# Performance work log

Measured on AMD Instinct MI355X. Metric: run time of the kernel, lower is better.

## Reference

```python
import jax, jax.numpy as jnp
import numpy as np

N, E, DIN, H, L, NCLS = 50000, 800000, 256, 384, 6, 2
EPS = 1e-5

def setup_inputs() -> dict:
    key = jax.random.key(0)
    ks = jax.random.split(key, 24)
    def lin(k, fan_in, shape):
        b = 1.0 / np.sqrt(fan_in)
        return jax.random.uniform(k, shape, jnp.float32, -b, b)
    inp = {}
    inp['x'] = jax.random.normal(ks[0], (N, DIN), jnp.float32)
    inp['edge_index'] = jax.random.randint(ks[1], (2, E), 0, N, jnp.int32)
    inp['W_in'] = lin(ks[2], DIN, (DIN, H)); inp['b_in'] = lin(ks[3], DIN, (H,))
    inp['bn0_g'] = jnp.ones((H,), jnp.float32); inp['bn0_b'] = jnp.zeros((H,), jnp.float32)
    inp['Wl'] = lin(ks[4], H, (L, H, H)); inp['bl'] = lin(ks[5], H, (L, H))
    inp['Wr'] = lin(ks[6], H, (L, H, H))
    inp['bn_g'] = jnp.ones((L, H), jnp.float32); inp['bn_b'] = jnp.zeros((L, H), jnp.float32)
    inp['Wskip'] = lin(ks[7], H, (L // 2, H, H)); inp['bskip'] = lin(ks[8], H, (L // 2, H))
    inp['W1'] = lin(ks[9], H, (H, H // 2)); inp['b1'] = lin(ks[10], H, (H // 2,))
    inp['W2'] = lin(ks[11], H // 2, (H // 2, H // 4)); inp['b2'] = lin(ks[12], H // 2, (H // 4,))
    inp['W3'] = lin(ks[13], H // 4, (H // 4, NCLS)); inp['b3'] = lin(ks[14], H // 4, (NCLS,))
    return inp

def _batchnorm(h, g, b):
    mu = jnp.mean(h, axis=0)
    var = jnp.mean(jnp.square(h - mu), axis=0)  # biased, as torch BN training
    return (h - mu) * jax.lax.rsqrt(var + EPS) * g + b

def reference(x, edge_index, W_in, b_in, bn0_g, bn0_b, Wl, bl, Wr, bn_g, bn_b,
              Wskip, bskip, W1, b1, W2, b2, W3, b3):
    row, col = edge_index[0], edge_index[1]  # messages flow row -> col
    cnt = jax.ops.segment_sum(jnp.ones((E,), jnp.float32), col, num_segments=N)
    inv_cnt = (1.0 / jnp.maximum(cnt, 1.0))[:, None]  # [N,1]

    h = _batchnorm(x @ W_in + b_in, bn0_g, bn0_b)
    h = jax.nn.relu(h)  # dropout is identity in eval

    skip_idx = 0
    for i in range(L):
        identity = h
        agg = jax.ops.segment_sum(h[row], col, num_segments=N) * inv_cnt  # mean aggregation
        h = agg @ Wl[i] + bl[i] + h @ Wr[i]  # SAGEConv: lin_l(mean) + lin_r(x)
        h = jax.nn.relu(_batchnorm(h, bn_g[i], bn_b[i]))
        if (i + 1) % 2 == 0 and skip_idx < L // 2:
            h = h + identity @ Wskip[skip_idx] + bskip[skip_idx]
            skip_idx += 1

    embeddings = h
    h = jax.nn.relu(h @ W1 + b1)
    h = jax.nn.relu(h @ W2 + b2)
    out = h @ W3 + b3
    return (out, embeddings)
```

## Files before the change

### kernel.cpp

```cpp
#include <hip/hip_runtime.h>

#define H 384
#define EPS 1e-5f

typedef __attribute__((ext_vector_type(8))) short bf8v;
typedef __attribute__((ext_vector_type(8))) unsigned short us8;
typedef __attribute__((ext_vector_type(4))) float f32x4;

__device__ __forceinline__ float b2f(unsigned short b) {
    return __builtin_bit_cast(float, (unsigned)b << 16);
}
__device__ __forceinline__ unsigned short f2b(float f) {
    unsigned u = __builtin_bit_cast(unsigned, f);
    u += 0x7FFFu + ((u >> 16) & 1u);
    return (unsigned short)(u >> 16);
}
__device__ __forceinline__ float u2f_lo(unsigned u) {
    return __builtin_bit_cast(float, u << 16);
}
__device__ __forceinline__ float u2f_hi(unsigned u) {
    return __builtin_bit_cast(float, u & 0xFFFF0000u);
}

__device__ __forceinline__ void gload16(const unsigned short* g, unsigned short* l) {
    __builtin_amdgcn_global_load_lds(
        (const __attribute__((address_space(1))) void*)g,
        (__attribute__((address_space(3))) void*)l, 16, 0, 0);
}

__global__ __launch_bounds__(256) void gemm_mfma(
    const unsigned short* __restrict__ A1, const unsigned short* __restrict__ W1t,
    const unsigned short* __restrict__ A2, const unsigned short* __restrict__ W2t,
    const float* __restrict__ bias, unsigned short* __restrict__ Cb,
    float* __restrict__ bnsum, float* __restrict__ bnsq,
    int Nr, int K, int M, int relu)
{
    __shared__ unsigned short smem[17408];
    __shared__ float s_stat[256];
    unsigned short* sA = smem;
    unsigned short* sB = smem + 8192;
    const int t = threadIdx.x;
    const int wave = t >> 6, lane = t & 63;
    const int wr = (wave >> 1) * 64, wc = (wave & 1) * 64;
    const int c0 = blockIdx.x * 128, r0 = blockIdx.y * 128;
    const int lm = lane & 15, lq = lane >> 4;
    const int l8 = lane >> 3;
    const int gsw8 = ((lane & 7) ^ l8) * 8;
    f32x4 acc[4][4] = {};

    s_stat[t] = 0.f;

    const int npass = (A2 != nullptr) ? 2 : 1;
    for (int pass = 0; pass < npass; ++pass) {
        const unsigned short* __restrict__ A = pass ? A2 : A1;
        const unsigned short* __restrict__ W = pass ? W2t : W1t;
        for (int k0 = 0; k0 < K; k0 += 64) {
            #pragma unroll
            for (int s = 0; s < 4; ++s) {
                const int seg = (wave << 2) + s;
                const int tr = (seg << 3) + l8;
                int gr = r0 + tr; if (gr >= Nr) gr = Nr - 1;
                gload16(A + (long)gr * K + k0 + gsw8, sA + (seg << 9));
                int gc = c0 + tr; if (gc >= M) gc = M - 1;
                gload16(W + (long)gc * K + k0 + gsw8, sB + (seg << 9));
            }
            __syncthreads();
            #pragma unroll
            for (int kk = 0; kk < 2; ++kk) {
                const int pc = (((kk << 2) | lq) ^ (lm & 7)) << 3;
                bf8v af[4], bf[4];
                #pragma unroll
                for (int i = 0; i < 4; ++i) {
                    const int ra = wr + (i << 4) + lm;
                    af[i] = *(const bf8v*)(sA + (ra << 6) + pc);
                    const int rb = wc + (i << 4) + lm;
                    bf[i] = *(const bf8v*)(sB + (rb << 6) + pc);
                }
                #pragma unroll
                for (int i = 0; i < 4; ++i)
                    #pragma unroll
                    for (int j = 0; j < 4; ++j)
                        acc[i][j] = __builtin_amdgcn_mfma_f32_16x16x32_bf16(
                            af[i], bf[j], acc[i][j], 0, 0, 0);
            }
            __syncthreads();
        }
    }

    const bool do_stats = (bnsum != nullptr);
    unsigned short* sC = smem;

    #pragma unroll
    for (int j = 0; j < 4; ++j) {
        const int lcol = wc + (j << 4) + lm;
        const int col = c0 + lcol;
        const float bi = (col < M) ? bias[col] : 0.f;
        float ls = 0.f, lss = 0.f;
        #pragma unroll
        for (int i = 0; i < 4; ++i) {
            const int lrow = wr + (i << 4) + (lq << 2);
            #pragma unroll
            for (int r = 0; r < 4; ++r) {
                float v = acc[i][j][r] + bi;
                if (r0 + lrow + r < Nr) { ls += v; lss += v * v; }
                sC[(lrow + r) * 136 + lcol] = f2b(relu ? fmaxf(v, 0.f) : v);
            }
        }
        if (do_stats && col < M) {
            atomicAdd(&s_stat[lcol], ls);
            atomicAdd(&s_stat[128 + lcol], lss);
        }
    }
    __syncthreads();
    if (do_stats && t < 128) {
        int col = c0 + t;
        if (col < M) {
            atomicAdd(&bnsum[col], s_stat[t]);
            atomicAdd(&bnsq[col], s_stat[128 + t]);
        }
    }
    #pragma unroll
    for (int it = 0; it < 8; ++it) {
        const int idx = (it << 8) + t;
        const int lrow = idx >> 4;
        const int ch = idx & 15;
        const int rowg = r0 + lrow;
        const int col = c0 + (ch << 3);
        if (rowg < Nr && col < M)
            *(bf8v*)(Cb + (long)rowg * M + col) =
                *(const bf8v*)(sC + lrow * 136 + (ch << 3));
    }
}

__global__ void wt_convert(const float* __restrict__ W, unsigned short* __restrict__ Wt,
                           int total, int K, int M)
{
    int idx = blockIdx.x * 256 + threadIdx.x;
    if (idx >= total) return;
    int l = idx / (K * M), rem = idx - l * K * M;
    int k = rem / M, m = rem - k * M;
    Wt[(long)l * K * M + (long)m * K + k] = f2b(W[idx]);
}

__global__ void f2b_vec(const float* __restrict__ X, unsigned short* __restrict__ Y, int n4)
{
    int idx = blockIdx.x * 256 + threadIdx.x;
    if (idx >= n4) return;
    float4 v = *(const float4*)(X + idx * 4);
    ushort4 o = {f2b(v.x), f2b(v.y), f2b(v.z), f2b(v.w)};
    *(ushort4*)(Y + idx * 4) = o;
}

__global__ void count_edges_i(const int* __restrict__ col, int* __restrict__ cnt, int E)
{
    int e = blockIdx.x * 256 + threadIdx.x;
    if (e < E) atomicAdd(&cnt[col[e]], 1);
}

__global__ __launch_bounds__(1024) void exscan_csr(const int* __restrict__ cnt,
                                                   int* __restrict__ offs, int n)
{
    __shared__ int s[1024];
    const int t = threadIdx.x;
    const int chunk = (n + 1023) >> 10;
    int lo = t * chunk, hi = lo + chunk;
    if (lo > n) lo = n;
    if (hi > n) hi = n;
    int sum = 0;
    for (int i = lo; i < hi; ++i) sum += cnt[i];
    s[t] = sum;
    __syncthreads();
    for (int d = 1; d < 1024; d <<= 1) {
        int o = (t >= d) ? s[t - d] : 0;
        __syncthreads();
        s[t] += o;
        __syncthreads();
    }
    int base = (t == 0) ? 0 : s[t - 1];
    for (int i = lo; i < hi; ++i) { offs[i] = base; base += cnt[i]; }
    if (t == 1023) offs[n] = s[1023];
}

__global__ void fill_csr(const int* __restrict__ row, const int* __restrict__ col,
                         const int* __restrict__ offs, int* __restrict__ cursor,
                         int* __restrict__ csr_rows, int E)
{
    int e = blockIdx.x * 256 + threadIdx.x;
    if (e < E) {
        int c = col[e];
        int p = offs[c] + atomicAdd(&cursor[c], 1);
        csr_rows[p] = row[e];
    }
}

__global__ void inv_from_cnt(const int* __restrict__ cnt, float* __restrict__ inv, int n)
{
    int i = blockIdx.x * 256 + threadIdx.x;
    if (i < n) inv[i] = 1.0f / fmaxf((float)cnt[i], 1.0f);
}

__global__ __launch_bounds__(256) void agg_gather(
    const unsigned short* __restrict__ hb, const int* __restrict__ csr_rows,
    const int* __restrict__ offs, const float* __restrict__ inv,
    unsigned short* __restrict__ aggb, int N)
{
    const int wave = threadIdx.x >> 6, lane = threadIdx.x & 63;
    const int node = blockIdx.x * 4 + wave;
    if (node >= N) return;
    const int lo = offs[node], hi = offs[node + 1];
    const int lofs = lane * 6;
    float s0 = 0.f, s1 = 0.f, s2 = 0.f, s3 = 0.f, s4 = 0.f, s5 = 0.f;
    int e = lo;
    for (; e + 7 < hi; e += 8) {
        uint3 v[8];
        #pragma unroll
        for (int q = 0; q < 8; ++q) {
            int r = __builtin_amdgcn_readfirstlane(csr_rows[e + q]);
            v[q] = *(const uint3*)(hb + (long)r * H + lofs);
        }
        #pragma unroll
        for (int q = 0; q < 8; ++q) {
            s0 += u2f_lo(v[q].x); s1 += u2f_hi(v[q].x);
            s2 += u2f_lo(v[q].y); s3 += u2f_hi(v[q].y);
            s4 += u2f_lo(v[q].z); s5 += u2f_hi(v[q].z);
        }
    }
    for (; e + 3 < hi; e += 4) {
        uint3 v[4];
        #pragma unroll
        for (int q = 0; q < 4; ++q) {
            int r = __builtin_amdgcn_readfirstlane(csr_rows[e + q]);
            v[q] = *(const uint3*)(hb + (long)r * H + lofs);
        }
        #pragma unroll
        for (int q = 0; q < 4; ++q) {
            s0 += u2f_lo(v[q].x); s1 += u2f_hi(v[q].x);
            s2 += u2f_lo(v[q].y); s3 += u2f_hi(v[q].y);
            s4 += u2f_lo(v[q].z); s5 += u2f_hi(v[q].z);
        }
    }
    for (; e < hi; ++e) {
        int r = __builtin_amdgcn_readfirstlane(csr_rows[e]);
        uint3 v = *(const uint3*)(hb + (long)r * H + lofs);
        s0 += u2f_lo(v.x); s1 += u2f_hi(v.x);
        s2 += u2f_lo(v.y); s3 += u2f_hi(v.y);
        s4 += u2f_lo(v.z); s5 += u2f_hi(v.z);
    }
    const float sc = inv[node];
    uint3 o;
    o.x = (unsigned)f2b(s0 * sc) | ((unsigned)f2b(s1 * sc) << 16);
    o.y = (unsigned)f2b(s2 * sc) | ((unsigned)f2b(s3 * sc) << 16);
    o.z = (unsigned)f2b(s4 * sc) | ((unsigned)f2b(s5 * sc) << 16);
    *(uint3*)(aggb + (long)node * H + lofs) = o;
}

__global__ __launch_bounds__(256) void bn_apply(
    const unsigned short* __restrict__ X, const float* __restrict__ bnsum,
    const float* __restrict__ bnsq, const float* __restrict__ g,
    const float* __restrict__ b, const unsigned short* __restrict__ S,
    unsigned short* __restrict__ outb, float* __restrict__ outf,
    int Nr, int total4)
{
    __shared__ float sc[H], sh[H];
    const int t = threadIdx.x;
    for (int j = t; j < H; j += 256) {
        float mu  = bnsum[j] / (float)Nr;
        float var = bnsq[j] / (float)Nr - mu * mu;
        float s   = g[j] * rsqrtf(fmaxf(var, 0.f) + EPS);
        sc[j] = s;
        sh[j] = b[j] - mu * s;
    }
    __syncthreads();
    int idx = blockIdx.x * 256 + t;
    if (idx >= total4) return;
    int base = idx * 4;
    int j = base % H;
    ushort4 v = *(const ushort4*)(X + base);
    float o0 = fmaxf(b2f(v.x) * sc[j + 0] + sh[j + 0], 0.f);
    float o1 = fmaxf(b2f(v.y) * sc[j + 1] + sh[j + 1], 0.f);
    float o2 = fmaxf(b2f(v.z) * sc[j + 2] + sh[j + 2], 0.f);
    float o3 = fmaxf(b2f(v.w) * sc[j + 3] + sh[j + 3], 0.f);
    if (S) {
        ushort4 s4 = *(const ushort4*)(S + base);
        o0 += b2f(s4.x); o1 += b2f(s4.y); o2 += b2f(s4.z); o3 += b2f(s4.w);
    }
    ushort4 o = {f2b(o0), f2b(o1), f2b(o2), f2b(o3)};
    *(ushort4*)(outb + base) = o;
    if (outf) {
        float4 of = {o0, o1, o2, o3};
        *(float4*)(outf + base) = of;
    }
}

__global__ void mlp3(const unsigned short* __restrict__ m2, const float* __restrict__ W3,
                     const float* __restrict__ b3, float* __restrict__ out, int N)
{
    int n = blockIdx.x * 256 + threadIdx.x;
    if (n >= N) return;
    float a0 = b3[0], a1 = b3[1];
    const unsigned short* r = m2 + (long)n * 96;
    #pragma unroll 4
    for (int k = 0; k < 96; ++k) {
        float v = b2f(r[k]);
        a0 += v * W3[k * 2];
        a1 += v * W3[k * 2 + 1];
    }
    out[n * 2 + 0] = a0;
    out[n * 2 + 1] = a1;
}

extern "C" void kernel_launch(void* const* d_in, const int* in_sizes, int n_in,
                              void* d_out, int out_size, void* d_ws, size_t ws_size,
                              hipStream_t stream)
{
    const float* x     = (const float*)d_in[0];
    const int*   ei    = (const int*)d_in[1];
    const float* W_in  = (const float*)d_in[2];
    const float* b_in  = (const float*)d_in[3];
    const float* bn0_g = (const float*)d_in[4];
    const float* bn0_b = (const float*)d_in[5];
    const float* Wl    = (const float*)d_in[6];
    const float* bl    = (const float*)d_in[7];
    const float* Wr    = (const float*)d_in[8];
    const float* bn_g  = (const float*)d_in[9];
    const float* bn_b  = (const float*)d_in[10];
    const float* Wskip = (const float*)d_in[11];
    const float* bskip = (const float*)d_in[12];
    const float* W1    = (const float*)d_in[13];
    const float* b1    = (const float*)d_in[14];
    const float* W2    = (const float*)d_in[15];
    const float* b2    = (const float*)d_in[16];
    const float* W3    = (const float*)d_in[17];
    const float* b3    = (const float*)d_in[18];

    const int DIN = 256;
    const int N = in_sizes[0] / DIN;
    const int E = in_sizes[1] / 2;
    const int* row = ei;
    const int* col = ei + E;
    const long NH = (long)N * H;

    unsigned short* tmp      = (unsigned short*)d_ws;
    unsigned short* hb       = tmp + NH;
    unsigned short* aggb     = hb + NH;
    unsigned short* Sbuf     = aggb + NH;
    unsigned short* xb       = Sbuf + NH;
    unsigned short* Wint     = xb + (long)N * DIN;
    unsigned short* Wlt      = Wint + (long)H * DIN;
    unsigned short* Wrt      = Wlt + 6L * H * H;
    unsigned short* Wskipt   = Wrt + 6L * H * H;
    unsigned short* W1t      = Wskipt + 3L * H * H;
    unsigned short* W2t      = W1t + 192L * H;
    float*          inv      = (float*)(W2t + 96L * 192);
    int*            offs     = (int*)(inv + N);
    int*            csr_rows = offs + (N + 1);
    int*            cnt      = csr_rows + E;
    int*            cursor   = cnt + N;
    float*          stats    = (float*)(cursor + N);
    float* out = (float*)d_out;
    float* emb = out + (long)N * 2;

    dim3 blk(256);
    const int rg128 = (N + 127) / 128;
    const int app_grid = (int)((NH / 4 + 255) / 256);

    hipMemsetAsync(cnt, 0, (2L * N + 14 * H) * sizeof(float), stream);

    count_edges_i<<<(E + 255) / 256, blk, 0, stream>>>(col, cnt, E);
    exscan_csr<<<1, 1024, 0, stream>>>(cnt, offs, N);
    inv_from_cnt<<<(N + 255) / 256, blk, 0, stream>>>(cnt, inv, N);
    fill_csr<<<(E + 255) / 256, blk, 0, stream>>>(row, col, offs, cursor, csr_rows, E);

    {
        int n1 = H * DIN;
        wt_convert<<<(n1 + 255) / 256, blk, 0, stream>>>(W_in, Wint, n1, DIN, H);
        int n2 = 6 * H * H;
        wt_convert<<<(n2 + 255) / 256, blk, 0, stream>>>(Wl, Wlt, n2, H, H);
        wt_convert<<<(n2 + 255) / 256, blk, 0, stream>>>(Wr, Wrt, n2, H, H);
        int n3 = 3 * H * H;
        wt_convert<<<(n3 + 255) / 256, blk, 0, stream>>>(Wskip, Wskipt, n3, H, H);
        int n4 = H * 192;
        wt_convert<<<(n4 + 255) / 256, blk, 0, stream>>>(W1, W1t, n4, H, 192);
        int n5 = 192 * 96;
        wt_convert<<<(n5 + 255) / 256, blk, 0, stream>>>(W2, W2t, n5, 192, 96);
    }

    {
        int n4 = N * DIN / 4;
        f2b_vec<<<(n4 + 255) / 256, blk, 0, stream>>>(x, xb, n4);
    }
    gemm_mfma<<<dim3(3, rg128), blk, 0, stream>>>(
        xb, Wint, nullptr, nullptr, b_in, tmp, stats, stats + H, N, DIN, H, 0);
    bn_apply<<<app_grid, blk, 0, stream>>>(
        tmp, stats, stats + H, bn0_g, bn0_b, nullptr, hb, nullptr, N, (int)(NH / 4));

    int skip_idx = 0;
    for (int i = 0; i < 6; ++i) {
        float* bs = stats + (i + 1) * 2 * H;
        agg_gather<<<(N + 3) / 4, blk, 0, stream>>>(hb, csr_rows, offs, inv, aggb, N);

        gemm_mfma<<<dim3(3, rg128), blk, 0, stream>>>(
            aggb, Wlt + (long)i * H * H, hb, Wrt + (long)i * H * H,
            bl + i * H, tmp, bs, bs + H, N, H, H, 0);

        const unsigned short* S = nullptr;
        if ((i & 1) == 1) {
            gemm_mfma<<<dim3(3, rg128), blk, 0, stream>>>(
                hb, Wskipt + (long)skip_idx * H * H, nullptr, nullptr,
                bskip + skip_idx * H, Sbuf, nullptr, nullptr, N, H, H, 0);
            skip_idx++;
            S = Sbuf;
        }
        bn_apply<<<app_grid, blk, 0, stream>>>(
            tmp, bs, bs + H, bn_g + i * H, bn_b + i * H, S, hb,
            (i == 5) ? emb : nullptr, N, (int)(NH / 4));
    }

    unsigned short* m1b = aggb;
    unsigned short* m2b = tmp;
    gemm_mfma<<<dim3(2, rg128), blk, 0, stream>>>(
        hb, W1t, nullptr, nullptr, b1, m1b, nullptr, nullptr, N, H, 192, 1);
    gemm_mfma<<<dim3(1, rg128), blk, 0, stream>>>(
        m1b, W2t, nullptr, nullptr, b2, m2b, nullptr, nullptr, N, 192, 96, 1);
    mlp3<<<(N + 255) / 256, blk, 0, stream>>>(m2b, W3, b3, out, N);
}
```

Baseline: 1.512 ms.

## Double-buffer GEMM k-tiles in LDS and vectorize final MLP layer loads

The MFMA GEMM moves from a single 64-wide k-tile buffer with two barriers per step to a double-buffered 32-wide k-tile pipeline. The next tile's global->LDS load is issued before computing the current one, with one barrier per step and a new XOR swizzle for the 32-column layout. The aim is to hide global load latency behind MFMA work, at the cost of twice as many loop iterations. Separately, mlp3 now caches W3 in shared memory and reads each row with 16-byte vector loads instead of scalar loads.

```diff
diff --git a/kernel.cpp b/kernel.cpp
--- a/kernel.cpp
+++ b/kernel.cpp
@@ -37,54 +37,56 @@
 {
     __shared__ unsigned short smem[17408];
     __shared__ float s_stat[256];
-    unsigned short* sA = smem;
-    unsigned short* sB = smem + 8192;
     const int t = threadIdx.x;
     const int wave = t >> 6, lane = t & 63;
     const int wr = (wave >> 1) * 64, wc = (wave & 1) * 64;
     const int c0 = blockIdx.x * 128, r0 = blockIdx.y * 128;
     const int lm = lane & 15, lq = lane >> 4;
-    const int l8 = lane >> 3;
-    const int gsw8 = ((lane & 7) ^ l8) * 8;
     f32x4 acc[4][4] = {};
 
     s_stat[t] = 0.f;
 
-    const int npass = (A2 != nullptr) ? 2 : 1;
-    for (int pass = 0; pass < npass; ++pass) {
-        const unsigned short* __restrict__ A = pass ? A2 : A1;
-        const unsigned short* __restrict__ W = pass ? W2t : W1t;
-        for (int k0 = 0; k0 < K; k0 += 64) {
+    const int K32 = K >> 5;
+    const int S = ((A2 != nullptr) ? 2 : 1) * K32;
+
+    auto stage = [&](int s, int b) {
+        const unsigned short* __restrict__ Ap = (s >= K32) ? A2 : A1;
+        const unsigned short* __restrict__ Wp = (s >= K32) ? W2t : W1t;
+        const int k0 = ((s >= K32) ? s - K32 : s) << 5;
+        unsigned short* Ab = smem + (b << 13);
+        #pragma unroll
+        for (int q = 0; q < 2; ++q) {
+            const int blk = (wave << 1) + q;
+            const int tr = (blk << 4) + (lane >> 2);
+            const int lc8 = (((lane & 3) ^ ((tr >> 1) & 3)) << 3);
+            int gr = r0 + tr; if (gr >= Nr) gr = Nr - 1;
+            gload16(Ap + (long)gr * K + k0 + lc8, Ab + (blk << 9));
+            int gc = c0 + tr; if (gc >= M) gc = M - 1;
+            gload16(Wp + (long)gc * K + k0 + lc8, Ab + 4096 + (blk << 9));
+        }
+    };
+
+    stage(0, 0);
+    __syncthreads();
+    for (int s = 0; s < S; ++s) {
+        const int cb = s & 1;
+        if (s + 1 < S) stage(s + 1, cb ^ 1);
+        const unsigned short* Ab = smem + (cb << 13);
+        bf8v af[4], bf[4];
+        #pragma unroll
+        for (int i = 0; i < 4; ++i) {
+            const int ra = wr + (i << 4) + lm;
+            af[i] = *(const bf8v*)(Ab + (ra << 5) + ((lq ^ ((ra >> 1) & 3)) << 3));
+            const int rb = wc + (i << 4) + lm;
+            bf[i] = *(const bf8v*)(Ab + 4096 + (rb << 5) + ((lq ^ ((rb >> 1) & 3)) << 3));
+        }
+        #pragma unroll
+        for (int i = 0; i < 4; ++i)
             #pragma unroll
-            for (int s = 0; s < 4; ++s) {
-                const int seg = (wave << 2) + s;
-                const int tr = (seg << 3) + l8;
-                int gr = r0 + tr; if (gr >= Nr) gr = Nr - 1;
-                gload16(A + (long)gr * K + k0 + gsw8, sA + (seg << 9));
-                int gc = c0 + tr; if (gc >= M) gc = M - 1;
-                gload16(W + (long)gc * K + k0 + gsw8, sB + (seg << 9));
-            }
-            __syncthreads();
-            #pragma unroll
-            for (int kk = 0; kk < 2; ++kk) {
-                const int pc = (((kk << 2) | lq) ^ (lm & 7)) << 3;
-                bf8v af[4], bf[4];
-                #pragma unroll
-                for (int i = 0; i < 4; ++i) {
-                    const int ra = wr + (i << 4) + lm;
-                    af[i] = *(const bf8v*)(sA + (ra << 6) + pc);
-                    const int rb = wc + (i << 4) + lm;
-                    bf[i] = *(const bf8v*)(sB + (rb << 6) + pc);
-                }
-                #pragma unroll
-                for (int i = 0; i < 4; ++i)
-                    #pragma unroll
-                    for (int j = 0; j < 4; ++j)
-                        acc[i][j] = __builtin_amdgcn_mfma_f32_16x16x32_bf16(
-                            af[i], bf[j], acc[i][j], 0, 0, 0);
-            }
-            __syncthreads();
-        }
+            for (int j = 0; j < 4; ++j)
+                acc[i][j] = __builtin_amdgcn_mfma_f32_16x16x32_bf16(
+                    af[i], bf[j], acc[i][j], 0, 0, 0);
+        __syncthreads();
     }
 
     const bool do_stats = (bnsum != nullptr);
@@ -292,18 +294,27 @@
     }
 }
 
-__global__ void mlp3(const unsigned short* __restrict__ m2, const float* __restrict__ W3,
-                     const float* __restrict__ b3, float* __restrict__ out, int N)
-{
-    int n = blockIdx.x * 256 + threadIdx.x;
+__global__ __launch_bounds__(256) void mlp3(
+    const unsigned short* __restrict__ m2, const float* __restrict__ W3,
+    const float* __restrict__ b3, float* __restrict__ out, int N)
+{
+    __shared__ float w[192];
+    const int t = threadIdx.x;
+    if (t < 192) w[t] = W3[t];
+    __syncthreads();
+    int n = blockIdx.x * 256 + t;
     if (n >= N) return;
     float a0 = b3[0], a1 = b3[1];
     const unsigned short* r = m2 + (long)n * 96;
-    #pragma unroll 4
-    for (int k = 0; k < 96; ++k) {
-        float v = b2f(r[k]);
-        a0 += v * W3[k * 2];
-        a1 += v * W3[k * 2 + 1];
+    #pragma unroll
+    for (int k8 = 0; k8 < 12; ++k8) {
+        us8 v = *(const us8*)(r + k8 * 8);
+        #pragma unroll
+        for (int q = 0; q < 8; ++q) {
+            float f = b2f(v[q]);
+            a0 += f * w[(k8 * 8 + q) * 2];
+            a1 += f * w[(k8 * 8 + q) * 2 + 1];
+        }
     }
     out[n * 2 + 0] = a0;
     out[n * 2 + 1] = a1;
```

Measured after the change: 1.573 ms. 1.04x slower.
